# Kernel tuning notes

Measured on AMD Instinct MI355X. Metric: run time of the kernel, lower is better.

## Reference

```python
import jax, jax.numpy as jnp
import numpy as np

N_NODES = 50000
N_EDGES = 800000
N_IN = 256
N_H = 64


def _xavier(key, fan_in, fan_out):
    limit = np.sqrt(6.0 / (fan_in + fan_out)).astype(np.float32)
    return jax.random.uniform(key, (fan_in, fan_out), jnp.float32, -limit, limit)


def setup_inputs() -> dict:
    key = jax.random.key(0)
    ks = jax.random.split(key, 12)
    inp = {
        "bf": jax.random.normal(ks[0], (1, N_NODES, N_IN), jnp.float32),
        "bl": jax.random.normal(ks[1], (1, N_NODES, N_IN), jnp.float32),
        "shuf_fts": jax.random.normal(ks[2], (1, N_NODES, N_IN), jnp.float32),
        "shuf_fls": jax.random.normal(ks[3], (1, N_NODES, N_IN), jnp.float32),
        "adj_rows": jax.random.randint(ks[4], (N_EDGES,), 0, N_NODES, jnp.int32),
        "adj_cols": jax.random.randint(ks[5], (N_EDGES,), 0, N_NODES, jnp.int32),
        "adj_w": jax.random.uniform(ks[6], (N_EDGES,), jnp.float32),
        "diff_rows": jax.random.randint(ks[7], (N_EDGES,), 0, N_NODES, jnp.int32),
        "diff_cols": jax.random.randint(ks[8], (N_EDGES,), 0, N_NODES, jnp.int32),
        "diff_w": jax.random.uniform(ks[9], (N_EDGES,), jnp.float32),
        # GCN parameters (Linear has bias=False; separate additive bias init 0; PReLU slope 0.25)
        "W1": _xavier(ks[10], N_IN, N_H),
        "b1": jnp.zeros((N_H,), jnp.float32),
        "a1": jnp.float32(0.25),
        "W2": _xavier(ks[11], N_IN, N_H),
        "b2": jnp.zeros((N_H,), jnp.float32),
        "a2": jnp.float32(0.25),
    }
    return inp


def _gcn(seq, W, b, a, rows, cols, w):
    # seq: [1, N, F_in]; sparse spmm: out[r] = sum_e 1[rows[e]==r] * w[e] * fts[cols[e]]
    fts = seq[0] @ W                                   # [N, n_h]
    msgs = w[:, None] * fts[cols]                      # [E, n_h] gather
    agg = jax.ops.segment_sum(msgs, rows, num_segments=N_NODES)  # [N, n_h] scatter-add
    out = agg[None, :, :] + b                          # bias add
    return jnp.where(out >= 0, out, a * out)           # PReLU


def reference(bf, bl, shuf_fts, shuf_fls, adj_rows, adj_cols, adj_w,
              diff_rows, diff_cols, diff_w, W1, b1, a1, W2, b2, a2):
    h_1 = _gcn(bf, W1, b1, a1, adj_rows, adj_cols, adj_w)
    h_2 = _gcn(bl, W2, b2, a2, diff_rows, diff_cols, diff_w)
    h_3 = _gcn(shuf_fts, W1, b1, a1, adj_rows, adj_cols, adj_w)
    h_4 = _gcn(shuf_fls, W2, b2, a2, diff_rows, diff_cols, diff_w)
    return jnp.stack([h_1, h_2, h_3, h_4])             # [4, 1, N, n_h]
```

## Files before the change

### kernel.cpp

```cpp
#include <hip/hip_runtime.h>
#include <hip/hip_bf16.h>

#define N_NODES 50000
#define N_EDGES 800000
#define N_IN    256
#define N_H     64
#define NB      125
#define RPB     400
#define BCAP    8192
#define EPT     8
#define BIN_BLK 2048
#define GSTRIDE 264

typedef short short8 __attribute__((ext_vector_type(8)));
typedef float f32x4  __attribute__((ext_vector_type(4)));

__device__ inline short f2bf(float f) {
    __bf16 h = (__bf16)f;
    return (short)__builtin_bit_cast(unsigned short, h);
}
__device__ inline float bflo(unsigned int q) { return __uint_as_float(q << 16); }
__device__ inline float bfhi(unsigned int q) { return __uint_as_float(q & 0xFFFF0000u); }


__global__ __launch_bounds__(256) void k_bin(
    const int* __restrict__ adj_rows, const int* __restrict__ adj_cols,
    const float* __restrict__ adj_w,
    const int* __restrict__ diff_rows, const int* __restrict__ diff_cols,
    const float* __restrict__ diff_w,
    int* __restrict__ gcnt, int2* __restrict__ bin) {

    int g = blockIdx.y;
    const int*   rows = g ? diff_rows : adj_rows;
    const int*   cols = g ? diff_cols : adj_cols;
    const float* ww   = g ? diff_w    : adj_w;
    int base_e = blockIdx.x * BIN_BLK;
    int t = threadIdx.x;

    __shared__ int lcnt[NB];
    __shared__ int lbase[NB];
    for (int i = t; i < NB; i += 256) lcnt[i] = 0;
    __syncthreads();

    int lpos[EPT];
    int bkt[EPT];
    #pragma unroll
    for (int e = 0; e < EPT; ++e) {
        int idx = base_e + e * 256 + t;
        if (idx < N_EDGES) {
            int r = rows[idx];
            int b = r / RPB;
            bkt[e] = b;
            lpos[e] = atomicAdd(&lcnt[b], 1);
        } else bkt[e] = -1;
    }
    __syncthreads();
    for (int i = t; i < NB; i += 256) lbase[i] = atomicAdd(&gcnt[g * NB + i], lcnt[i]);
    __syncthreads();

    #pragma unroll
    for (int e = 0; e < EPT; ++e) {
        int idx = base_e + e * 256 + t;
        if (idx < N_EDGES) {
            unsigned int r = (unsigned int)rows[idx];
            unsigned int c = (unsigned int)cols[idx];
            int b = bkt[e];
            int2 m;
            m.x = (int)((r << 16) | c);
            m.y = __float_as_int(ww[idx]);
            bin[((size_t)(g * NB + b)) * BCAP + lbase[b] + lpos[e]] = m;
        }
    }
}


__global__ __launch_bounds__(256) void k_build(
    const int* __restrict__ gcnt, const int2* __restrict__ bin,
    int2* __restrict__ csr, int* __restrict__ row_ptr) {

    int g = blockIdx.y, b = blockIdx.x, t = threadIdx.x;
    __shared__ int hist[512];
    __shared__ int s2[256];
    __shared__ int sbase;

    for (int i = t; i < 512; i += 256) hist[i] = 0;
    __syncthreads();

    int cnt = gcnt[g * NB + b];
    const int2* be = bin + ((size_t)(g * NB + b)) * BCAP;
    int r0 = b * RPB;

    for (int i = t; i < cnt; i += 256) {
        unsigned int rc = (unsigned int)be[i].x;
        atomicAdd(&hist[(rc >> 16) - r0], 1);
    }
    __syncthreads();

    if (t == 0) {
        int s = 0;
        for (int i = 0; i < b; ++i) s += gcnt[g * NB + i];
        sbase = s;
    }

    int v0 = hist[2 * t], v1 = hist[2 * t + 1];
    int local = v0 + v1;
    s2[t] = local;
    __syncthreads();
    for (int off = 1; off < 256; off <<= 1) {
        int v = (t >= off) ? s2[t - off] : 0;
        __syncthreads();
        s2[t] += v;
        __syncthreads();
    }
    int e0 = sbase + (s2[t] - local);
    int e1 = e0 + v0;

    int* rp = row_ptr + g * (N_NODES + 1);
    if (2 * t < RPB)     rp[r0 + 2 * t]     = e0;
    if (2 * t + 1 < RPB) rp[r0 + 2 * t + 1] = e1;
    __syncthreads();
    hist[2 * t] = e0;
    hist[2 * t + 1] = e1;
    __syncthreads();

    int2* cg = csr + (size_t)g * N_EDGES;
    for (int i = t; i < cnt; i += 256) {
        int2 m = be[i];
        unsigned int rc = (unsigned int)m.x;
        int lr = (int)(rc >> 16) - r0;
        int pos = atomicAdd(&hist[lr], 1);
        int2 o;
        o.x = (int)(rc & 0xFFFFu);
        o.y = m.y;
        cg[pos] = o;
    }
    if (b == NB - 1 && t == 0) rp[N_NODES] = N_EDGES;
}


__global__ __launch_bounds__(256) void k_wt(const float* __restrict__ W1,
                                            const float* __restrict__ W2,
                                            unsigned short* __restrict__ WTg) {
    int g = blockIdx.x;
    const float* W = g ? W2 : W1;
    unsigned short* o = WTg + (size_t)g * 64 * GSTRIDE;
    for (int i = threadIdx.x; i < N_IN * N_H; i += 256) {
        int k = i >> 6, c = i & 63;
        o[c * GSTRIDE + k] = (unsigned short)f2bf(W[i]);
    }
}


__global__ __launch_bounds__(512, 4) void k_gemm(
    const float* __restrict__ X0, const float* __restrict__ X1,
    const float* __restrict__ X2, const float* __restrict__ X3,
    const unsigned short* __restrict__ WTg,
    unsigned short* __restrict__ Tadj, unsigned short* __restrict__ Tdiff) {

    int g = blockIdx.y;
    unsigned short* T = g ? Tdiff : Tadj;
    const unsigned short* src = WTg + (size_t)g * 64 * GSTRIDE;

    __shared__ __align__(16) unsigned short WT[64 * GSTRIDE];
    {
        const uint4* s4 = (const uint4*)src;
        uint4* d4 = (uint4*)WT;
        int t = threadIdx.x;
        #pragma unroll
        for (int j = 0; j < 3; ++j) d4[t + 512 * j] = s4[t + 512 * j];
        d4[t + 1536] = s4[t + 1536];
        if (t < 64) d4[2048 + t] = s4[2048 + t];
    }
    __syncthreads();

    int wid  = threadIdx.x >> 6;
    int lane = threadIdx.x & 63;
    int s    = wid & 1;
    int rb   = blockIdx.x * 64 + (wid >> 1) * 16;
    if (rb >= N_NODES) return;

    const float* X = s ? (g ? X3 : X2) : (g ? X1 : X0);
    int coloff = s * 64;

    int arow = rb + (lane & 15);
    if (arow >= N_NODES) arow = N_NODES - 1;
    int kg   = lane >> 4;
    const float4* p = reinterpret_cast<const float4*>(X + (size_t)arow * N_IN) + kg * 2;

    float4 rx[16];
    #pragma unroll
    for (int kt = 0; kt < 8; ++kt) {
        rx[2 * kt]     = p[kt * 8];
        rx[2 * kt + 1] = p[kt * 8 + 1];
    }

    f32x4 acc[4];
    #pragma unroll
    for (int ct = 0; ct < 4; ++ct) acc[ct] = (f32x4){0.f, 0.f, 0.f, 0.f};

    #pragma unroll
    for (int kt = 0; kt < 8; ++kt) {
        float4 a0 = rx[2 * kt];
        float4 a1 = rx[2 * kt + 1];
        short8 af;
        af[0] = f2bf(a0.x); af[1] = f2bf(a0.y); af[2] = f2bf(a0.z); af[3] = f2bf(a0.w);
        af[4] = f2bf(a1.x); af[5] = f2bf(a1.y); af[6] = f2bf(a1.z); af[7] = f2bf(a1.w);
        #pragma unroll
        for (int ct = 0; ct < 4; ++ct) {
            const unsigned short* wp = &WT[(ct * 16 + (lane & 15)) * GSTRIDE + kt * 32 + kg * 8];
            short8 bfr = *reinterpret_cast<const short8*>(wp);
            acc[ct] = __builtin_amdgcn_mfma_f32_16x16x32_bf16(af, bfr, acc[ct], 0, 0, 0);
        }
    }

    int rgrp = lane >> 4;
    #pragma unroll
    for (int ct = 0; ct < 4; ++ct) {
        int col = coloff + ct * 16 + (lane & 15);
        #pragma unroll
        for (int r = 0; r < 4; ++r) {
            int row = rb + rgrp * 4 + r;
            if (row < N_NODES)
                T[(size_t)row * 128 + col] = (unsigned short)f2bf(acc[ct][r]);
        }
    }
}


__global__ __launch_bounds__(256) void k_agg(
    const int* __restrict__ row_ptr, const int2* __restrict__ csr,
    const unsigned int* __restrict__ Tadj, const unsigned int* __restrict__ Tdiff,
    const float* __restrict__ b1, const float* __restrict__ a1,
    const float* __restrict__ b2, const float* __restrict__ a2,
    float* __restrict__ out) {

    int wid  = threadIdx.x >> 6;
    int lane = threadIdx.x & 63;
    int node = blockIdx.x * 4 + wid;
    int g    = blockIdx.y;

    const int* rp = row_ptr + g * (N_NODES + 1);
    const int2* el = csr + (size_t)g * N_EDGES;
    const unsigned int* Tu = g ? Tdiff : Tadj;

    int e  = rp[node];
    int e1 = rp[node + 1];
    float ax = 0.f, ay = 0.f;

    for (; e + 4 <= e1; e += 4) {
        int2 m0 = el[e + 0], m1 = el[e + 1], m2 = el[e + 2], m3 = el[e + 3];
        unsigned int q0 = Tu[(size_t)m0.x * 64 + lane];
        unsigned int q1 = Tu[(size_t)m1.x * 64 + lane];
        unsigned int q2 = Tu[(size_t)m2.x * 64 + lane];
        unsigned int q3 = Tu[(size_t)m3.x * 64 + lane];
        float w0 = __int_as_float(m0.y), w1 = __int_as_float(m1.y);
        float w2 = __int_as_float(m2.y), w3 = __int_as_float(m3.y);
        ax += w0 * bflo(q0); ay += w0 * bfhi(q0);
        ax += w1 * bflo(q1); ay += w1 * bfhi(q1);
        ax += w2 * bflo(q2); ay += w2 * bfhi(q2);
        ax += w3 * bflo(q3); ay += w3 * bfhi(q3);
    }
    for (; e < e1; ++e) {
        int2 m = el[e];
        unsigned int q = Tu[(size_t)m.x * 64 + lane];
        float w = __int_as_float(m.y);
        ax += w * bflo(q); ay += w * bfhi(q);
    }

    const float* bias = g ? b2 : b1;
    float slope = g ? a2[0] : a1[0];
    int f = 2 * lane;
    size_t base;
    int fo;
    if (lane < 32) { base = g ? (size_t)3200000 : (size_t)0;       fo = f; }
    else           { base = g ? (size_t)9600000 : (size_t)6400000; fo = f - 64; }
    float v0 = ax + bias[fo];
    float v1 = ay + bias[fo + 1];
    v0 = (v0 >= 0.f) ? v0 : slope * v0;
    v1 = (v1 >= 0.f) ? v1 : slope * v1;
    float2 res; res.x = v0; res.y = v1;
    *reinterpret_cast<float2*>(out + base + (size_t)node * 64 + fo) = res;
}


extern "C" void kernel_launch(void* const* d_in, const int* in_sizes, int n_in,
                              void* d_out, int out_size, void* d_ws, size_t ws_size,
                              hipStream_t stream) {
    const float* bf_      = (const float*)d_in[0];
    const float* bl_      = (const float*)d_in[1];
    const float* shuf_fts = (const float*)d_in[2];
    const float* shuf_fls = (const float*)d_in[3];
    const int*   adj_rows = (const int*)d_in[4];
    const int*   adj_cols = (const int*)d_in[5];
    const float* adj_w    = (const float*)d_in[6];
    const int*   diff_rows= (const int*)d_in[7];
    const int*   diff_cols= (const int*)d_in[8];
    const float* diff_w   = (const float*)d_in[9];
    const float* W1       = (const float*)d_in[10];
    const float* b1       = (const float*)d_in[11];
    const float* a1       = (const float*)d_in[12];
    const float* W2       = (const float*)d_in[13];
    const float* b2       = (const float*)d_in[14];
    const float* a2       = (const float*)d_in[15];
    float* out = (float*)d_out;

    char* ws = (char*)d_ws;
    unsigned short* Tadj  = (unsigned short*)(ws);
    unsigned short* Tdiff = (unsigned short*)(ws + 12800000);
    int2* csr             = (int2*)(ws + 25600000);
    int*  row_ptr         = (int*)(ws + 38400000);
    int*  gcnt            = (int*)(ws + 38801024);
    unsigned short* WTg   = (unsigned short*)(ws + 38803072);

    int2* bin = (int2*)d_out;

    hipMemsetAsync(gcnt, 0, 2 * NB * sizeof(int), stream);

    k_bin<<<dim3((N_EDGES + BIN_BLK - 1) / BIN_BLK, 2), dim3(256), 0, stream>>>(
        adj_rows, adj_cols, adj_w, diff_rows, diff_cols, diff_w, gcnt, bin);
    k_wt<<<dim3(2), dim3(256), 0, stream>>>(W1, W2, WTg);
    k_build<<<dim3(NB, 2), dim3(256), 0, stream>>>(gcnt, bin, csr, row_ptr);

    k_gemm<<<dim3((N_NODES + 63) / 64, 2), dim3(512), 0, stream>>>(
        bf_, bl_, shuf_fts, shuf_fls, WTg, Tadj, Tdiff);

    k_agg<<<dim3(N_NODES / 4, 2), dim3(256), 0, stream>>>(
        row_ptr, csr, (const unsigned int*)Tadj, (const unsigned int*)Tdiff,
        b1, a1, b2, a2, out);
}
```

Measured before the change: 209.5 us.

## Restructure GEMM to stage activations in LDS and keep weights in registers

The projection GEMM now uses 32-row tiles with 256 threads and one grid slot per (graph, input). Each block loads its fp32 activation rows with coalesced float4 reads, converts them to bf16 and stores them in shared memory. Each wave keeps its weight fragments in registers, loaded straight from global memory, so the shared-memory copy of the full weight matrix is gone. This is meant to improve global load coalescing and reduce shared-memory use so more blocks fit per CU, at the cost of more blocks, more registers per thread, and an extra barrier.

```diff
diff --git a/kernel.cpp b/kernel.cpp
--- a/kernel.cpp
+++ b/kernel.cpp
@@ -10,7 +10,8 @@
 #define BCAP    8192
 #define EPT     8
 #define BIN_BLK 2048
-#define GSTRIDE 264
+#define GSTRIDE 256
+#define ASTRIDE 264
 
 typedef short short8 __attribute__((ext_vector_type(8)));
 typedef float f32x4  __attribute__((ext_vector_type(4)));
@@ -151,77 +152,101 @@
 }
 
 
-__global__ __launch_bounds__(512, 4) void k_gemm(
+__global__ __launch_bounds__(256, 4) void k_gemm(
     const float* __restrict__ X0, const float* __restrict__ X1,
     const float* __restrict__ X2, const float* __restrict__ X3,
     const unsigned short* __restrict__ WTg,
     unsigned short* __restrict__ Tadj, unsigned short* __restrict__ Tdiff) {
 
-    int g = blockIdx.y;
+    int gy = blockIdx.y;
+    int g = gy >> 1, s = gy & 1;
+    const float* X = g ? (s ? X3 : X1) : (s ? X2 : X0);
     unsigned short* T = g ? Tdiff : Tadj;
-    const unsigned short* src = WTg + (size_t)g * 64 * GSTRIDE;
-
-    __shared__ __align__(16) unsigned short WT[64 * GSTRIDE];
-    {
-        const uint4* s4 = (const uint4*)src;
-        uint4* d4 = (uint4*)WT;
-        int t = threadIdx.x;
+    const unsigned short* WB = WTg + (size_t)g * 64 * GSTRIDE;
+    int coloff = s * 64;
+
+    int t    = threadIdx.x;
+    int wid  = t >> 6;
+    int lane = t & 63;
+    int l15  = lane & 15;
+    int kg   = lane >> 4;
+    int rb0  = blockIdx.x * 32;
+
+    __shared__ __align__(16) unsigned short A[32 * ASTRIDE];
+
+    float4 v[4];
+    #pragma unroll
+    for (int j = 0; j < 4; ++j) {
+        int idx = t + 256 * j;
+        int row = idx >> 6, col4 = idx & 63;
+        int grow = rb0 + row; if (grow >= N_NODES) grow = N_NODES - 1;
+        v[j] = ((const float4*)(X + (size_t)grow * N_IN))[col4];
+    }
+
+    int ctbase = (wid >> 1) * 2;
+    short8 bfr[2][8];
+    #pragma unroll
+    for (int c2 = 0; c2 < 2; ++c2) {
+        int ct = ctbase + c2;
         #pragma unroll
-        for (int j = 0; j < 3; ++j) d4[t + 512 * j] = s4[t + 512 * j];
-        d4[t + 1536] = s4[t + 1536];
-        if (t < 64) d4[2048 + t] = s4[2048 + t];
-    }
-    __syncthreads();
-
-    int wid  = threadIdx.x >> 6;
-    int lane = threadIdx.x & 63;
-    int s    = wid & 1;
-    int rb   = blockIdx.x * 64 + (wid >> 1) * 16;
-    if (rb >= N_NODES) return;
-
-    const float* X = s ? (g ? X3 : X2) : (g ? X1 : X0);
-    int coloff = s * 64;
-
-    int arow = rb + (lane & 15);
-    if (arow >= N_NODES) arow = N_NODES - 1;
-    int kg   = lane >> 4;
-    const float4* p = reinterpret_cast<const float4*>(X + (size_t)arow * N_IN) + kg * 2;
-
-    float4 rx[16];
+        for (int kt = 0; kt < 8; ++kt) {
+            bfr[c2][kt] = *reinterpret_cast<const short8*>(
+                WB + ((ct * 16 + l15) * GSTRIDE + kt * 32 + kg * 8));
+        }
+    }
+
+    #pragma unroll
+    for (int j = 0; j < 4; ++j) {
+        int idx = t + 256 * j;
+        int row = idx >> 6, col4 = idx & 63;
+        ushort4 c;
+        c.x = (unsigned short)f2bf(v[j].x);
+        c.y = (unsigned short)f2bf(v[j].y);
+        c.z = (unsigned short)f2bf(v[j].z);
+        c.w = (unsigned short)f2bf(v[j].w);
+        *reinterpret_cast<ushort4*>(&A[row * ASTRIDE + col4 * 4]) = c;
+    }
+    #pragma unroll
+    for (int j = 4; j < 8; ++j) {
+        int idx = t + 256 * j;
+        int row = idx >> 6, col4 = idx & 63;
+        int grow = rb0 + row; if (grow >= N_NODES) grow = N_NODES - 1;
+        v[j - 4] = ((const float4*)(X + (size_t)grow * N_IN))[col4];
+    }
+    #pragma unroll
+    for (int j = 4; j < 8; ++j) {
+        int idx = t + 256 * j;
+        int row = idx >> 6, col4 = idx & 63;
+        ushort4 c;
+        c.x = (unsigned short)f2bf(v[j - 4].x);
+        c.y = (unsigned short)f2bf(v[j - 4].y);
+        c.z = (unsigned short)f2bf(v[j - 4].z);
+        c.w = (unsigned short)f2bf(v[j - 4].w);
+        *reinterpret_cast<ushort4*>(&A[row * ASTRIDE + col4 * 4]) = c;
+    }
+    __syncthreads();
+
+    int rt = wid & 1;
+    f32x4 acc[2];
+    acc[0] = (f32x4){0.f, 0.f, 0.f, 0.f};
+    acc[1] = (f32x4){0.f, 0.f, 0.f, 0.f};
+
     #pragma unroll
     for (int kt = 0; kt < 8; ++kt) {
-        rx[2 * kt]     = p[kt * 8];
-        rx[2 * kt + 1] = p[kt * 8 + 1];
-    }
-
-    f32x4 acc[4];
-    #pragma unroll
-    for (int ct = 0; ct < 4; ++ct) acc[ct] = (f32x4){0.f, 0.f, 0.f, 0.f};
-
-    #pragma unroll
-    for (int kt = 0; kt < 8; ++kt) {
-        float4 a0 = rx[2 * kt];
-        float4 a1 = rx[2 * kt + 1];
-        short8 af;
-        af[0] = f2bf(a0.x); af[1] = f2bf(a0.y); af[2] = f2bf(a0.z); af[3] = f2bf(a0.w);
-        af[4] = f2bf(a1.x); af[5] = f2bf(a1.y); af[6] = f2bf(a1.z); af[7] = f2bf(a1.w);
-        #pragma unroll
-        for (int ct = 0; ct < 4; ++ct) {
-            const unsigned short* wp = &WT[(ct * 16 + (lane & 15)) * GSTRIDE + kt * 32 + kg * 8];
-            short8 bfr = *reinterpret_cast<const short8*>(wp);
-            acc[ct] = __builtin_amdgcn_mfma_f32_16x16x32_bf16(af, bfr, acc[ct], 0, 0, 0);
-        }
-    }
-
-    int rgrp = lane >> 4;
-    #pragma unroll
-    for (int ct = 0; ct < 4; ++ct) {
-        int col = coloff + ct * 16 + (lane & 15);
+        short8 af = *reinterpret_cast<const short8*>(
+            &A[(rt * 16 + l15) * ASTRIDE + kt * 32 + kg * 8]);
+        acc[0] = __builtin_amdgcn_mfma_f32_16x16x32_bf16(af, bfr[0][kt], acc[0], 0, 0, 0);
+        acc[1] = __builtin_amdgcn_mfma_f32_16x16x32_bf16(af, bfr[1][kt], acc[1], 0, 0, 0);
+    }
+
+    #pragma unroll
+    for (int c2 = 0; c2 < 2; ++c2) {
+        int col = coloff + (ctbase + c2) * 16 + l15;
         #pragma unroll
         for (int r = 0; r < 4; ++r) {
-            int row = rb + rgrp * 4 + r;
+            int row = rb0 + rt * 16 + kg * 4 + r;
             if (row < N_NODES)
-                T[(size_t)row * 128 + col] = (unsigned short)f2bf(acc[ct][r]);
+                T[(size_t)row * 128 + col] = (unsigned short)f2bf(acc[c2][r]);
         }
     }
 }
@@ -321,7 +346,7 @@
     k_wt<<<dim3(2), dim3(256), 0, stream>>>(W1, W2, WTg);
     k_build<<<dim3(NB, 2), dim3(256), 0, stream>>>(gcnt, bin, csr, row_ptr);
 
-    k_gemm<<<dim3((N_NODES + 63) / 64, 2), dim3(512), 0, stream>>>(
+    k_gemm<<<dim3((N_NODES + 31) / 32, 4), dim3(256), 0, stream>>>(
         bf_, bl_, shuf_fts, shuf_fls, WTg, Tadj, Tdiff);
 
     k_agg<<<dim3(N_NODES / 4, 2), dim3(256), 0, stream>>>(
```

New measurement: 225.6 us. 1.08x slower.
